# Kernel tuning notes

Measured on AMD Instinct MI355X. Metric: run time of the kernel, lower is better.

Reference implementation:

```python
import jax, jax.numpy as jnp
import numpy as np

B, T, IN, H, STEPS = 32768, 11, 2, 64, 80


def gru_cell(x, h, W_ih, W_hh, b_ih, b_hh):
    # PyTorch GRU cell: gates ordered (r, z, n)
    gi = x @ W_ih.T + b_ih            # [B, 3H]
    gh = h @ W_hh.T + b_hh            # [B, 3H]
    gi_r, gi_z, gi_n = jnp.split(gi, 3, axis=-1)
    gh_r, gh_z, gh_n = jnp.split(gh, 3, axis=-1)
    r = jax.nn.sigmoid(gi_r + gh_r)
    z = jax.nn.sigmoid(gi_z + gh_z)
    n = jnp.tanh(gi_n + r * gh_n)
    return (1.0 - z) * n + z * h


def setup_inputs() -> dict:
    key = jax.random.key(0)
    ks = jax.random.split(key, 20)
    s = 1.0 / np.sqrt(H)
    u = lambda k, shape: jax.random.uniform(k, shape, jnp.float32, -s, s)
    inp = {"x": jax.random.normal(ks[0], (B, T, IN), jnp.float32)}
    i = 1
    for pfx, in0 in (("e", IN), ("d", IN)):
        for l, d_in in ((0, in0), (1, H)):
            inp[f"{pfx}W_ih{l}"] = u(ks[i], (3 * H, d_in)); i += 1
            inp[f"{pfx}W_hh{l}"] = u(ks[i], (3 * H, H)); i += 1
            inp[f"{pfx}b_ih{l}"] = u(ks[i], (3 * H,)); i += 1
            inp[f"{pfx}b_hh{l}"] = u(ks[i], (3 * H,)); i += 1
    inp["fc_W"] = u(ks[17], (2, H))
    inp["fc_b"] = u(ks[18], (2,))
    return inp


def reference(x, eW_ih0, eW_hh0, eb_ih0, eb_hh0, eW_ih1, eW_hh1, eb_ih1, eb_hh1,
              dW_ih0, dW_hh0, db_ih0, db_hh0, dW_ih1, dW_hh1, db_ih1, db_hh1,
              fc_W, fc_b):
    b = x.shape[0]
    h0 = jnp.zeros((b, H), x.dtype)
    h1 = jnp.zeros((b, H), x.dtype)

    # ---- encoder: 2-layer GRU over time (dropout inactive in eval) ----
    def enc_step(carry, xt):
        c0, c1 = carry
        c0 = gru_cell(xt, c0, eW_ih0, eW_hh0, eb_ih0, eb_hh0)
        c1 = gru_cell(c0, c1, eW_ih1, eW_hh1, eb_ih1, eb_hh1)
        return (c0, c1), None

    (h0, h1), _ = jax.lax.scan(enc_step, (h0, h1), jnp.swapaxes(x, 0, 1))

    def dec_step(carry, _):
        inp, c0, c1 = carry
        c0 = gru_cell(inp, c0, dW_ih0, dW_hh0, db_ih0, db_hh0)
        c1 = gru_cell(c0, c1, dW_ih1, dW_hh1, db_ih1, db_hh1)
        pred = c1 @ fc_W.T + fc_b     # [B, 2]
        return (pred, c0, c1), pred

    init = (x[:, -1, :], h0, h1)
    _, preds = jax.lax.scan(dec_step, init, None, length=STEPS)  # [80, B, 2]
    return jnp.swapaxes(preds, 0, 1)  # [B, 80, 2]
```

## Files before the change

kernel.cpp:

```cpp
#include <hip/hip_runtime.h>
#include <cstddef>

#define T_SEQ 11
#define STEPS 80
#define SRC (-1.44269504f)
#define SNC ( 2.88539008f)

typedef _Float16 f16;
typedef _Float16 f16x4 __attribute__((ext_vector_type(4)));
typedef _Float16 f16x8 __attribute__((ext_vector_type(8)));
typedef float    f32x4 __attribute__((ext_vector_type(4)));

#define W0H   0
#define W1X   12288
#define WPADO 24576
#define HB    30720
#define BIASH 47104
#define LDS_BYTES (47104*2 + 512*4)

__device__ __forceinline__ f32x4 mfma16(f16x8 a, f16x8 b, f32x4 c) {
    return __builtin_amdgcn_mfma_f32_16x16x32_f16(a, b, c, 0, 0, 0);
}

__device__ __forceinline__ void stage_w(f16* lds, int dst, const float* __restrict__ W, int tid) {
    for (int c = tid; c < 1536; c += 512) {
        const int row = c >> 3, kc = c & 7;
        const float sc = (row < 128) ? SRC : SNC;
        const float* p = W + row * 64 + kc * 8;
        f16x8 v;
        #pragma unroll
        for (int i = 0; i < 8; ++i) v[i] = (f16)(sc * p[i]);
        *(f16x8*)(lds + dst + row * 64 + ((kc ^ (row & 7)) << 3)) = v;
    }
}
__device__ __forceinline__ void stage_pad(f16* lds, const float* __restrict__ Wih0, int tid) {
    for (int c = tid; c < 768; c += 512) {
        const int row = c >> 2, kc = c & 3;
        const float sc = (row < 128) ? SRC : SNC;
        f16x8 v;
        #pragma unroll
        for (int i = 0; i < 8; ++i) v[i] = (f16)0.f;
        if (kc == 0) { v[0] = (f16)(sc * Wih0[row * 2]); v[1] = (f16)(sc * Wih0[row * 2 + 1]); }
        *(f16x8*)(lds + WPADO + row * 32 + ((kc ^ (row & 3)) << 3)) = v;
    }
}
__device__ __forceinline__ void stage_bias(float* bb, int base, const float* __restrict__ bih,
                                           const float* __restrict__ bhh, int tid) {
    for (int t = tid; t < 256; t += 512) {
        const int a = t >> 6, j = t & 63;
        float v;
        if (a == 0)      v = SRC * (bih[j] + bhh[j]);
        else if (a == 1) v = SRC * (bih[64 + j] + bhh[64 + j]);
        else if (a == 2) v = SNC * bih[128 + j];
        else             v = SNC * bhh[128 + j];
        bb[(base + a) * 64 + j] = v;
    }
}

__device__ __forceinline__ f16x8 wfrag(const float* __restrict__ W, int row, int k0, float sc) {
    f16x8 r;
    #pragma unroll
    for (int i = 0; i < 8; ++i) r[i] = (f16)(sc * W[row * 64 + k0 + i]);
    return r;
}
__device__ __forceinline__ void load_wregs(f16x8 (&R)[8], f16x8 (&Z)[8], f16x8 (&N)[8],
                                           const float* __restrict__ Whh, int col, int quad) {
    #pragma unroll
    for (int ks = 0; ks < 2; ++ks) {
        #pragma unroll
        for (int mt = 0; mt < 4; ++mt) {
            const int k0 = ks * 32 + quad * 8;
            R[ks * 4 + mt] = wfrag(Whh, mt * 16 + col,       k0, SRC);
            Z[ks * 4 + mt] = wfrag(Whh, 64  + mt * 16 + col, k0, SRC);
            N[ks * 4 + mt] = wfrag(Whh, 128 + mt * 16 + col, k0, SNC);
        }
    }
}

struct Lane {
    int col, quad, c7, colr, x0, x1, xp;
    int wo[4];
};

__device__ __forceinline__ void cell_l0(f16* lds, const Lane& L, f16x4 (&ho)[4],
                                        f16x8 xpb, int h0off)
{
    const float* bb = (const float*)(lds + BIASH);
    f16x8 hb0 = *(const f16x8*)(lds + h0off + L.colr + L.x0);
    f16x8 hb1 = *(const f16x8*)(lds + h0off + L.colr + L.x1);
    #pragma unroll
    for (int mt = 0; mt < 4; ++mt) {
        const int bj = mt * 16 + L.quad * 4;
        f32x4 bR  = *(const f32x4*)(bb + 0 * 64 + bj);
        f32x4 bZ  = *(const f32x4*)(bb + 1 * 64 + bj);
        f32x4 bNi = *(const f32x4*)(bb + 2 * 64 + bj);
        f32x4 bNh = *(const f32x4*)(bb + 3 * 64 + bj);
        const int ar = (mt * 16 + L.col) * 64;
        f16x8 hR0 = *(const f16x8*)(lds + W0H        + ar + L.x0);
        f16x8 hR1 = *(const f16x8*)(lds + W0H        + ar + L.x1);
        f16x8 hZ0 = *(const f16x8*)(lds + W0H + 4096 + ar + L.x0);
        f16x8 hZ1 = *(const f16x8*)(lds + W0H + 4096 + ar + L.x1);
        f16x8 hN0 = *(const f16x8*)(lds + W0H + 8192 + ar + L.x0);
        f16x8 hN1 = *(const f16x8*)(lds + W0H + 8192 + ar + L.x1);
        const int pr = (mt * 16 + L.col) * 32;
        f16x8 pR = *(const f16x8*)(lds + WPADO        + pr + L.xp);
        f16x8 pZ = *(const f16x8*)(lds + WPADO + 2048 + pr + L.xp);
        f16x8 pN = *(const f16x8*)(lds + WPADO + 4096 + pr + L.xp);
        f32x4 aR  = mfma16(hR0, hb0, bR);  aR  = mfma16(hR1, hb1, aR);
        f32x4 aZ  = mfma16(hZ0, hb0, bZ);  aZ  = mfma16(hZ1, hb1, aZ);
        f32x4 aNh = mfma16(hN0, hb0, bNh); aNh = mfma16(hN1, hb1, aNh);
        aR  = mfma16(pR, xpb, aR);
        aZ  = mfma16(pZ, xpb, aZ);
        f32x4 aNi = mfma16(pN, xpb, bNi);
        f16x4 o;
        #pragma unroll
        for (int i = 0; i < 4; ++i) {
            const float r = __builtin_amdgcn_rcpf(1.f + __builtin_amdgcn_exp2f(aR[i]));
            const float z = __builtin_amdgcn_rcpf(1.f + __builtin_amdgcn_exp2f(aZ[i]));
            const float n = 1.f - 2.f * __builtin_amdgcn_rcpf(1.f + __builtin_amdgcn_exp2f(aNi[i] + r * aNh[i]));
            const float h = n + z * ((float)ho[mt][i] - n);
            o[i] = (f16)h;
        }
        ho[mt] = o;
        *(f16x4*)(lds + h0off + L.wo[mt]) = o;
    }
}

__device__ __forceinline__ void cell_l1(f16* lds, const Lane& L, f16x4 (&ho)[4],
    const f16x8 (&cR)[8], const f16x8 (&cZ)[8], const f16x8 (&cN)[8],
    int h0off, int h1off)
{
    const float* bb = (const float*)(lds + BIASH);
    f16x8 xb0 = *(const f16x8*)(lds + h0off + L.colr + L.x0);
    f16x8 xb1 = *(const f16x8*)(lds + h0off + L.colr + L.x1);
    f16x8 hb0 = *(const f16x8*)(lds + h1off + L.colr + L.x0);
    f16x8 hb1 = *(const f16x8*)(lds + h1off + L.colr + L.x1);
    #pragma unroll
    for (int mt = 0; mt < 4; ++mt) {
        const int bj = mt * 16 + L.quad * 4;
        f32x4 bR  = *(const f32x4*)(bb + 4 * 64 + bj);
        f32x4 bZ  = *(const f32x4*)(bb + 5 * 64 + bj);
        f32x4 bNi = *(const f32x4*)(bb + 6 * 64 + bj);
        f32x4 bNh = *(const f32x4*)(bb + 7 * 64 + bj);
        const int ar = (mt * 16 + L.col) * 64;
        f16x8 xR0 = *(const f16x8*)(lds + W1X        + ar + L.x0);
        f16x8 xR1 = *(const f16x8*)(lds + W1X        + ar + L.x1);
        f16x8 xZ0 = *(const f16x8*)(lds + W1X + 4096 + ar + L.x0);
        f16x8 xZ1 = *(const f16x8*)(lds + W1X + 4096 + ar + L.x1);
        f16x8 xN0 = *(const f16x8*)(lds + W1X + 8192 + ar + L.x0);
        f16x8 xN1 = *(const f16x8*)(lds + W1X + 8192 + ar + L.x1);
        f32x4 aR  = mfma16(cR[mt],     hb0, bR);
        f32x4 aZ  = mfma16(cZ[mt],     hb0, bZ);
        f32x4 aNh = mfma16(cN[mt],     hb0, bNh);
        aR  = mfma16(cR[4 + mt], hb1, aR);
        aZ  = mfma16(cZ[4 + mt], hb1, aZ);
        aNh = mfma16(cN[4 + mt], hb1, aNh);
        aR  = mfma16(xR0, xb0, aR);   aR  = mfma16(xR1, xb1, aR);
        aZ  = mfma16(xZ0, xb0, aZ);   aZ  = mfma16(xZ1, xb1, aZ);
        f32x4 aNi = mfma16(xN0, xb0, bNi); aNi = mfma16(xN1, xb1, aNi);
        f16x4 o;
        #pragma unroll
        for (int i = 0; i < 4; ++i) {
            const float r = __builtin_amdgcn_rcpf(1.f + __builtin_amdgcn_exp2f(aR[i]));
            const float z = __builtin_amdgcn_rcpf(1.f + __builtin_amdgcn_exp2f(aZ[i]));
            const float n = 1.f - 2.f * __builtin_amdgcn_rcpf(1.f + __builtin_amdgcn_exp2f(aNi[i] + r * aNh[i]));
            const float h = n + z * ((float)ho[mt][i] - n);
            o[i] = (f16)h;
        }
        ho[mt] = o;
        *(f16x4*)(lds + h1off + L.wo[mt]) = o;
    }
}

__global__ __launch_bounds__(512, 1)
void gru_wave3(
    const float* __restrict__ x,
    const float* __restrict__ eWih0, const float* __restrict__ eWhh0,
    const float* __restrict__ ebih0, const float* __restrict__ ebhh0,
    const float* __restrict__ eWih1, const float* __restrict__ eWhh1,
    const float* __restrict__ ebih1, const float* __restrict__ ebhh1,
    const float* __restrict__ dWih0, const float* __restrict__ dWhh0,
    const float* __restrict__ dbih0, const float* __restrict__ dbhh0,
    const float* __restrict__ dWih1, const float* __restrict__ dWhh1,
    const float* __restrict__ dbih1, const float* __restrict__ dbhh1,
    const float* __restrict__ fcW,  const float* __restrict__ fcb,
    float* __restrict__ out)
{
    extern __shared__ f16 lds[];
    float* bb = (float*)(lds + BIASH);
    const int tid  = threadIdx.x;
    const int lane = tid & 63;
    const int wv   = __builtin_amdgcn_readfirstlane(tid >> 6);

    Lane L;
    L.col  = lane & 15;
    L.quad = lane >> 4;
    L.c7   = L.col & 7;
    L.colr = L.col * 64;
    L.x0   = (L.quad ^ L.c7) << 3;
    L.x1   = ((4 + L.quad) ^ L.c7) << 3;
    L.xp   = (L.quad ^ (L.col & 3)) << 3;
    #pragma unroll
    for (int mt = 0; mt < 4; ++mt)
        L.wo[mt] = L.colr + (((2 * mt + (L.quad >> 1)) ^ L.c7) << 3) + ((L.quad & 1) << 2);

    const int r0    = blockIdx.x * 128;
    const int myrow = r0 + wv * 16 + L.col;
    const int h0off = HB + wv * 2048;
    const int h1off = h0off + 1024;

    stage_w(lds, W0H, eWhh0, tid);
    stage_w(lds, W1X, eWih1, tid);
    stage_pad(lds, eWih0, tid);
    stage_bias(bb, 0, ebih0, ebhh0, tid);
    stage_bias(bb, 4, ebih1, ebhh1, tid);
    {
        f16x8 z;
        #pragma unroll
        for (int i = 0; i < 8; ++i) z[i] = (f16)0.f;
        for (int k = lane; k < 256; k += 64) *(f16x8*)(lds + h0off + k * 8) = z;
    }
    f16x8 w1R[8], w1Z[8], w1N[8];
    load_wregs(w1R, w1Z, w1N, eWhh1, L.col, L.quad);
    f16x4 ho0[4], ho1[4];
    #pragma unroll
    for (int m = 0; m < 4; ++m) {
        #pragma unroll
        for (int i = 0; i < 4; ++i) { ho0[m][i] = (f16)0.f; ho1[m][i] = (f16)0.f; }
    }
    __syncthreads();

    const float* xrow = x + (size_t)myrow * (T_SEQ * 2);
    f16x8 zf;
    #pragma unroll
    for (int i = 0; i < 8; ++i) zf[i] = (f16)0.f;

    #pragma unroll 1
    for (int t = 0; t < T_SEQ; ++t) {
        const float2 xv = *(const float2*)(xrow + t * 2);
        f16x8 xpb = zf;
        if (L.quad == 0) { xpb[0] = (f16)xv.x; xpb[1] = (f16)xv.y; }
        cell_l0(lds, L, ho0, xpb, h0off);
        cell_l1(lds, L, ho1, w1R, w1Z, w1N, h0off, h1off);
    }

    __syncthreads();
    stage_w(lds, W0H, dWhh0, tid);
    stage_w(lds, W1X, dWih1, tid);
    stage_pad(lds, dWih0, tid);
    stage_bias(bb, 0, dbih0, dbhh0, tid);
    stage_bias(bb, 4, dbih1, dbhh1, tid);
    load_wregs(w1R, w1Z, w1N, dWhh1, L.col, L.quad);
    __syncthreads();

    f16x8 fcf0 = zf, fcf1 = zf;
    if (L.col < 2) {
        #pragma unroll
        for (int i = 0; i < 8; ++i) {
            fcf0[i] = (f16)fcW[L.col * 64 + L.quad * 8 + i];
            fcf1[i] = (f16)fcW[L.col * 64 + 32 + L.quad * 8 + i];
        }
    }
    f32x4 pb;
    #pragma unroll
    for (int rg = 0; rg < 4; ++rg) pb[rg] = (L.quad == 0 && rg < 2) ? fcb[rg] : 0.f;

    float* __restrict__ outp = out + (size_t)myrow * (STEPS * 2);

    f16x8 xpb = zf;
    {
        const float2 xv = *(const float2*)(xrow + (T_SEQ - 1) * 2);
        if (L.quad == 0) { xpb[0] = (f16)xv.x; xpb[1] = (f16)xv.y; }
    }

    #pragma unroll 1
    for (int s = 0; s < STEPS; ++s) {
        cell_l0(lds, L, ho0, xpb, h0off);
        cell_l1(lds, L, ho1, w1R, w1Z, w1N, h0off, h1off);
        f16x8 b0 = *(const f16x8*)(lds + h1off + L.colr + L.x0);
        f16x8 b1 = *(const f16x8*)(lds + h1off + L.colr + L.x1);
        f32x4 p = mfma16(fcf0, b0, pb);
        p = mfma16(fcf1, b1, p);
        xpb = zf;
        if (L.quad == 0) {
            *(float2*)(outp + s * 2) = make_float2(p[0], p[1]);
            xpb[0] = (f16)p[0];
            xpb[1] = (f16)p[1];
        }
    }
}

extern "C" void kernel_launch(void* const* d_in, const int* in_sizes, int n_in,
                              void* d_out, int out_size, void* d_ws, size_t ws_size,
                              hipStream_t stream) {
    (void)n_in; (void)out_size; (void)d_ws; (void)ws_size;

    const float* x     = (const float*)d_in[0];
    const float* eWih0 = (const float*)d_in[1];
    const float* eWhh0 = (const float*)d_in[2];
    const float* ebih0 = (const float*)d_in[3];
    const float* ebhh0 = (const float*)d_in[4];
    const float* eWih1 = (const float*)d_in[5];
    const float* eWhh1 = (const float*)d_in[6];
    const float* ebih1 = (const float*)d_in[7];
    const float* ebhh1 = (const float*)d_in[8];
    const float* dWih0 = (const float*)d_in[9];
    const float* dWhh0 = (const float*)d_in[10];
    const float* dbih0 = (const float*)d_in[11];
    const float* dbhh0 = (const float*)d_in[12];
    const float* dWih1 = (const float*)d_in[13];
    const float* dWhh1 = (const float*)d_in[14];
    const float* dbih1 = (const float*)d_in[15];
    const float* dbhh1 = (const float*)d_in[16];
    const float* fcW   = (const float*)d_in[17];
    const float* fcb   = (const float*)d_in[18];
    float* out = (float*)d_out;

    hipFuncSetAttribute((const void*)gru_wave3,
        hipFuncAttributeMaxDynamicSharedMemorySize, LDS_BYTES);

    const int b = in_sizes[0] / (T_SEQ * 2);
    dim3 grid(b / 128), block(512);
    hipLaunchKernelGGL(gru_wave3, grid, block, LDS_BYTES, stream,
        x, eWih0, eWhh0, ebih0, ebhh0, eWih1, eWhh1, ebih1, ebhh1,
        dWih0, dWhh0, dbih0, dbhh0, dWih1, dWhh1, dbih1, dbhh1,
        fcW, fcb, out);
}
```

Before: 480.9 us.

## Process two 16-row tiles per wave and keep layer-1 input weights in registers

Each wave now handles 32 batch rows as two 16-row N-tiles, so every weight fragment read from LDS feeds two MFMA chains. The block shrinks from 8 to 4 waves (256 threads) while still covering 128 rows. Layer-1 input weights move from LDS into registers alongside the recurrent weights, which frees LDS and removes those per-step LDS reads. This doubles register pressure for weights and state and halves the waves per CU, so there is less latency hiding and a risk of spills.

```diff
diff --git a/kernel.cpp b/kernel.cpp
--- a/kernel.cpp
+++ b/kernel.cpp
@@ -12,18 +12,17 @@
 typedef float    f32x4 __attribute__((ext_vector_type(4)));
 
 #define W0H   0
-#define W1X   12288
-#define WPADO 24576
-#define HB    30720
-#define BIASH 47104
-#define LDS_BYTES (47104*2 + 512*4)
+#define WPADO 12288
+#define HB    18432
+#define BIASH 34816
+#define LDS_BYTES (34816*2 + 512*4)
 
 __device__ __forceinline__ f32x4 mfma16(f16x8 a, f16x8 b, f32x4 c) {
     return __builtin_amdgcn_mfma_f32_16x16x32_f16(a, b, c, 0, 0, 0);
 }
 
 __device__ __forceinline__ void stage_w(f16* lds, int dst, const float* __restrict__ W, int tid) {
-    for (int c = tid; c < 1536; c += 512) {
+    for (int c = tid; c < 1536; c += 256) {
         const int row = c >> 3, kc = c & 7;
         const float sc = (row < 128) ? SRC : SNC;
         const float* p = W + row * 64 + kc * 8;
@@ -34,7 +33,7 @@
     }
 }
 __device__ __forceinline__ void stage_pad(f16* lds, const float* __restrict__ Wih0, int tid) {
-    for (int c = tid; c < 768; c += 512) {
+    for (int c = tid; c < 768; c += 256) {
         const int row = c >> 2, kc = c & 3;
         const float sc = (row < 128) ? SRC : SNC;
         f16x8 v;
@@ -46,7 +45,7 @@
 }
 __device__ __forceinline__ void stage_bias(float* bb, int base, const float* __restrict__ bih,
                                            const float* __restrict__ bhh, int tid) {
-    for (int t = tid; t < 256; t += 512) {
+    for (int t = tid; t < 256; t += 256) {
         const int a = t >> 6, j = t & 63;
         float v;
         if (a == 0)      v = SRC * (bih[j] + bhh[j]);
@@ -64,15 +63,15 @@
     return r;
 }
 __device__ __forceinline__ void load_wregs(f16x8 (&R)[8], f16x8 (&Z)[8], f16x8 (&N)[8],
-                                           const float* __restrict__ Whh, int col, int quad) {
+                                           const float* __restrict__ W, int col, int quad) {
     #pragma unroll
     for (int ks = 0; ks < 2; ++ks) {
         #pragma unroll
         for (int mt = 0; mt < 4; ++mt) {
             const int k0 = ks * 32 + quad * 8;
-            R[ks * 4 + mt] = wfrag(Whh, mt * 16 + col,       k0, SRC);
-            Z[ks * 4 + mt] = wfrag(Whh, 64  + mt * 16 + col, k0, SRC);
-            N[ks * 4 + mt] = wfrag(Whh, 128 + mt * 16 + col, k0, SNC);
+            R[ks * 4 + mt] = wfrag(W, mt * 16 + col,       k0, SRC);
+            Z[ks * 4 + mt] = wfrag(W, 64  + mt * 16 + col, k0, SRC);
+            N[ks * 4 + mt] = wfrag(W, 128 + mt * 16 + col, k0, SNC);
         }
     }
 }
@@ -82,12 +81,32 @@
     int wo[4];
 };
 
-__device__ __forceinline__ void cell_l0(f16* lds, const Lane& L, f16x4 (&ho)[4],
-                                        f16x8 xpb, int h0off)
+__device__ __forceinline__ void gates4(f32x4 aR, f32x4 aZ, f32x4 aNi, f32x4 aNh,
+                                       f16x4& ho, f16* dst)
+{
+    f16x4 o;
+    #pragma unroll
+    for (int i = 0; i < 4; ++i) {
+        const float r = __builtin_amdgcn_rcpf(1.f + __builtin_amdgcn_exp2f(aR[i]));
+        const float z = __builtin_amdgcn_rcpf(1.f + __builtin_amdgcn_exp2f(aZ[i]));
+        const float n = 1.f - 2.f * __builtin_amdgcn_rcpf(1.f + __builtin_amdgcn_exp2f(aNi[i] + r * aNh[i]));
+        const float h = n + z * ((float)ho[i] - n);
+        o[i] = (f16)h;
+    }
+    ho = o;
+    *(f16x4*)dst = o;
+}
+
+__device__ __forceinline__ void cell_l0(f16* lds, const Lane& L, f16x4 (&ho)[4][2],
+                                        const f16x8 (&xpb)[2], int h0b)
 {
     const float* bb = (const float*)(lds + BIASH);
-    f16x8 hb0 = *(const f16x8*)(lds + h0off + L.colr + L.x0);
-    f16x8 hb1 = *(const f16x8*)(lds + h0off + L.colr + L.x1);
+    f16x8 hb[2][2];
+    #pragma unroll
+    for (int nt = 0; nt < 2; ++nt) {
+        hb[nt][0] = *(const f16x8*)(lds + h0b + nt * 1024 + L.colr + L.x0);
+        hb[nt][1] = *(const f16x8*)(lds + h0b + nt * 1024 + L.colr + L.x1);
+    }
     #pragma unroll
     for (int mt = 0; mt < 4; ++mt) {
         const int bj = mt * 16 + L.quad * 4;
@@ -106,35 +125,33 @@
         f16x8 pR = *(const f16x8*)(lds + WPADO        + pr + L.xp);
         f16x8 pZ = *(const f16x8*)(lds + WPADO + 2048 + pr + L.xp);
         f16x8 pN = *(const f16x8*)(lds + WPADO + 4096 + pr + L.xp);
-        f32x4 aR  = mfma16(hR0, hb0, bR);  aR  = mfma16(hR1, hb1, aR);
-        f32x4 aZ  = mfma16(hZ0, hb0, bZ);  aZ  = mfma16(hZ1, hb1, aZ);
-        f32x4 aNh = mfma16(hN0, hb0, bNh); aNh = mfma16(hN1, hb1, aNh);
-        aR  = mfma16(pR, xpb, aR);
-        aZ  = mfma16(pZ, xpb, aZ);
-        f32x4 aNi = mfma16(pN, xpb, bNi);
-        f16x4 o;
-        #pragma unroll
-        for (int i = 0; i < 4; ++i) {
-            const float r = __builtin_amdgcn_rcpf(1.f + __builtin_amdgcn_exp2f(aR[i]));
-            const float z = __builtin_amdgcn_rcpf(1.f + __builtin_amdgcn_exp2f(aZ[i]));
-            const float n = 1.f - 2.f * __builtin_amdgcn_rcpf(1.f + __builtin_amdgcn_exp2f(aNi[i] + r * aNh[i]));
-            const float h = n + z * ((float)ho[mt][i] - n);
-            o[i] = (f16)h;
-        }
-        ho[mt] = o;
-        *(f16x4*)(lds + h0off + L.wo[mt]) = o;
-    }
-}
-
-__device__ __forceinline__ void cell_l1(f16* lds, const Lane& L, f16x4 (&ho)[4],
+        #pragma unroll
+        for (int nt = 0; nt < 2; ++nt) {
+            f32x4 aR  = mfma16(hR0, hb[nt][0], bR);  aR  = mfma16(hR1, hb[nt][1], aR);
+            f32x4 aZ  = mfma16(hZ0, hb[nt][0], bZ);  aZ  = mfma16(hZ1, hb[nt][1], aZ);
+            f32x4 aNh = mfma16(hN0, hb[nt][0], bNh); aNh = mfma16(hN1, hb[nt][1], aNh);
+            aR = mfma16(pR, xpb[nt], aR);
+            aZ = mfma16(pZ, xpb[nt], aZ);
+            f32x4 aNi = mfma16(pN, xpb[nt], bNi);
+            gates4(aR, aZ, aNi, aNh, ho[mt][nt], lds + h0b + nt * 1024 + L.wo[mt]);
+        }
+    }
+}
+
+__device__ __forceinline__ void cell_l1(f16* lds, const Lane& L, f16x4 (&ho)[4][2],
     const f16x8 (&cR)[8], const f16x8 (&cZ)[8], const f16x8 (&cN)[8],
-    int h0off, int h1off)
+    const f16x8 (&xR)[8], const f16x8 (&xZ)[8], const f16x8 (&xN)[8],
+    int h0b, int h1b)
 {
     const float* bb = (const float*)(lds + BIASH);
-    f16x8 xb0 = *(const f16x8*)(lds + h0off + L.colr + L.x0);
-    f16x8 xb1 = *(const f16x8*)(lds + h0off + L.colr + L.x1);
-    f16x8 hb0 = *(const f16x8*)(lds + h1off + L.colr + L.x0);
-    f16x8 hb1 = *(const f16x8*)(lds + h1off + L.colr + L.x1);
+    f16x8 xb[2][2], hv[2][2];
+    #pragma unroll
+    for (int nt = 0; nt < 2; ++nt) {
+        xb[nt][0] = *(const f16x8*)(lds + h0b + nt * 1024 + L.colr + L.x0);
+        xb[nt][1] = *(const f16x8*)(lds + h0b + nt * 1024 + L.colr + L.x1);
+        hv[nt][0] = *(const f16x8*)(lds + h1b + nt * 1024 + L.colr + L.x0);
+        hv[nt][1] = *(const f16x8*)(lds + h1b + nt * 1024 + L.colr + L.x1);
+    }
     #pragma unroll
     for (int mt = 0; mt < 4; ++mt) {
         const int bj = mt * 16 + L.quad * 4;
@@ -142,38 +159,27 @@
         f32x4 bZ  = *(const f32x4*)(bb + 5 * 64 + bj);
         f32x4 bNi = *(const f32x4*)(bb + 6 * 64 + bj);
         f32x4 bNh = *(const f32x4*)(bb + 7 * 64 + bj);
-        const int ar = (mt * 16 + L.col) * 64;
-        f16x8 xR0 = *(const f16x8*)(lds + W1X        + ar + L.x0);
-        f16x8 xR1 = *(const f16x8*)(lds + W1X        + ar + L.x1);
-        f16x8 xZ0 = *(const f16x8*)(lds + W1X + 4096 + ar + L.x0);
-        f16x8 xZ1 = *(const f16x8*)(lds + W1X + 4096 + ar + L.x1);
-        f16x8 xN0 = *(const f16x8*)(lds + W1X + 8192 + ar + L.x0);
-        f16x8 xN1 = *(const f16x8*)(lds + W1X + 8192 + ar + L.x1);
-        f32x4 aR  = mfma16(cR[mt],     hb0, bR);
-        f32x4 aZ  = mfma16(cZ[mt],     hb0, bZ);
-        f32x4 aNh = mfma16(cN[mt],     hb0, bNh);
-        aR  = mfma16(cR[4 + mt], hb1, aR);
-        aZ  = mfma16(cZ[4 + mt], hb1, aZ);
-        aNh = mfma16(cN[4 + mt], hb1, aNh);
-        aR  = mfma16(xR0, xb0, aR);   aR  = mfma16(xR1, xb1, aR);
-        aZ  = mfma16(xZ0, xb0, aZ);   aZ  = mfma16(xZ1, xb1, aZ);
-        f32x4 aNi = mfma16(xN0, xb0, bNi); aNi = mfma16(xN1, xb1, aNi);
-        f16x4 o;
-        #pragma unroll
-        for (int i = 0; i < 4; ++i) {
-            const float r = __builtin_amdgcn_rcpf(1.f + __builtin_amdgcn_exp2f(aR[i]));
-            const float z = __builtin_amdgcn_rcpf(1.f + __builtin_amdgcn_exp2f(aZ[i]));
-            const float n = 1.f - 2.f * __builtin_amdgcn_rcpf(1.f + __builtin_amdgcn_exp2f(aNi[i] + r * aNh[i]));
-            const float h = n + z * ((float)ho[mt][i] - n);
-            o[i] = (f16)h;
-        }
-        ho[mt] = o;
-        *(f16x4*)(lds + h1off + L.wo[mt]) = o;
-    }
-}
-
-__global__ __launch_bounds__(512, 1)
-void gru_wave3(
+        #pragma unroll
+        for (int nt = 0; nt < 2; ++nt) {
+            f32x4 aR  = mfma16(cR[mt], hv[nt][0], bR);
+            f32x4 aZ  = mfma16(cZ[mt], hv[nt][0], bZ);
+            f32x4 aNh = mfma16(cN[mt], hv[nt][0], bNh);
+            aR  = mfma16(cR[4 + mt], hv[nt][1], aR);
+            aZ  = mfma16(cZ[4 + mt], hv[nt][1], aZ);
+            aNh = mfma16(cN[4 + mt], hv[nt][1], aNh);
+            aR  = mfma16(xR[mt], xb[nt][0], aR);
+            aZ  = mfma16(xZ[mt], xb[nt][0], aZ);
+            f32x4 aNi = mfma16(xN[mt], xb[nt][0], bNi);
+            aR  = mfma16(xR[4 + mt], xb[nt][1], aR);
+            aZ  = mfma16(xZ[4 + mt], xb[nt][1], aZ);
+            aNi = mfma16(xN[4 + mt], xb[nt][1], aNi);
+            gates4(aR, aZ, aNi, aNh, ho[mt][nt], lds + h1b + nt * 1024 + L.wo[mt]);
+        }
+    }
+}
+
+__global__ __launch_bounds__(256, 1)
+void gru_wave4(
     const float* __restrict__ x,
     const float* __restrict__ eWih0, const float* __restrict__ eWhh0,
     const float* __restrict__ ebih0, const float* __restrict__ ebhh0,
@@ -204,13 +210,11 @@
     for (int mt = 0; mt < 4; ++mt)
         L.wo[mt] = L.colr + (((2 * mt + (L.quad >> 1)) ^ L.c7) << 3) + ((L.quad & 1) << 2);
 
-    const int r0    = blockIdx.x * 128;
-    const int myrow = r0 + wv * 16 + L.col;
-    const int h0off = HB + wv * 2048;
-    const int h1off = h0off + 1024;
+    const int rowb = blockIdx.x * 128 + wv * 32;
+    const int h0b  = HB + wv * 4096;
+    const int h1b  = h0b + 2048;
 
     stage_w(lds, W0H, eWhh0, tid);
-    stage_w(lds, W1X, eWih1, tid);
     stage_pad(lds, eWih0, tid);
     stage_bias(bb, 0, ebih0, ebhh0, tid);
     stage_bias(bb, 4, ebih1, ebhh1, tid);
@@ -218,39 +222,49 @@
         f16x8 z;
         #pragma unroll
         for (int i = 0; i < 8; ++i) z[i] = (f16)0.f;
-        for (int k = lane; k < 256; k += 64) *(f16x8*)(lds + h0off + k * 8) = z;
-    }
-    f16x8 w1R[8], w1Z[8], w1N[8];
-    load_wregs(w1R, w1Z, w1N, eWhh1, L.col, L.quad);
-    f16x4 ho0[4], ho1[4];
+        for (int k = lane; k < 512; k += 64) *(f16x8*)(lds + h0b + k * 8) = z;
+    }
+    f16x8 c1R[8], c1Z[8], c1N[8];
+    f16x8 x1R[8], x1Z[8], x1N[8];
+    load_wregs(c1R, c1Z, c1N, eWhh1, L.col, L.quad);
+    load_wregs(x1R, x1Z, x1N, eWih1, L.col, L.quad);
+    f16x4 ho0[4][2], ho1[4][2];
     #pragma unroll
     for (int m = 0; m < 4; ++m) {
         #pragma unroll
-        for (int i = 0; i < 4; ++i) { ho0[m][i] = (f16)0.f; ho1[m][i] = (f16)0.f; }
+        for (int nt = 0; nt < 2; ++nt) {
+            #pragma unroll
+            for (int i = 0; i < 4; ++i) { ho0[m][nt][i] = (f16)0.f; ho1[m][nt][i] = (f16)0.f; }
+        }
     }
     __syncthreads();
 
-    const float* xrow = x + (size_t)myrow * (T_SEQ * 2);
+    const float* xr0 = x + (size_t)(rowb + L.col) * (T_SEQ * 2);
+    const float* xr1 = x + (size_t)(rowb + 16 + L.col) * (T_SEQ * 2);
     f16x8 zf;
     #pragma unroll
     for (int i = 0; i < 8; ++i) zf[i] = (f16)0.f;
 
     #pragma unroll 1
     for (int t = 0; t < T_SEQ; ++t) {
-        const float2 xv = *(const float2*)(xrow + t * 2);
-        f16x8 xpb = zf;
-        if (L.quad == 0) { xpb[0] = (f16)xv.x; xpb[1] = (f16)xv.y; }
-        cell_l0(lds, L, ho0, xpb, h0off);
-        cell_l1(lds, L, ho1, w1R, w1Z, w1N, h0off, h1off);
+        f16x8 xpb[2] = {zf, zf};
+        if (L.quad == 0) {
+            const float2 a = *(const float2*)(xr0 + t * 2);
+            const float2 b = *(const float2*)(xr1 + t * 2);
+            xpb[0][0] = (f16)a.x; xpb[0][1] = (f16)a.y;
+            xpb[1][0] = (f16)b.x; xpb[1][1] = (f16)b.y;
+        }
+        cell_l0(lds, L, ho0, xpb, h0b);
+        cell_l1(lds, L, ho1, c1R, c1Z, c1N, x1R, x1Z, x1N, h0b, h1b);
     }
 
     __syncthreads();
     stage_w(lds, W0H, dWhh0, tid);
-    stage_w(lds, W1X, dWih1, tid);
     stage_pad(lds, dWih0, tid);
     stage_bias(bb, 0, dbih0, dbhh0, tid);
     stage_bias(bb, 4, dbih1, dbhh1, tid);
-    load_wregs(w1R, w1Z, w1N, dWhh1, L.col, L.quad);
+    load_wregs(c1R, c1Z, c1N, dWhh1, L.col, L.quad);
+    load_wregs(x1R, x1Z, x1N, dWih1, L.col, L.quad);
     __syncthreads();
 
     f16x8 fcf0 = zf, fcf1 = zf;
@@ -265,27 +279,34 @@
     #pragma unroll
     for (int rg = 0; rg < 4; ++rg) pb[rg] = (L.quad == 0 && rg < 2) ? fcb[rg] : 0.f;
 
-    float* __restrict__ outp = out + (size_t)myrow * (STEPS * 2);
-
-    f16x8 xpb = zf;
-    {
-        const float2 xv = *(const float2*)(xrow + (T_SEQ - 1) * 2);
-        if (L.quad == 0) { xpb[0] = (f16)xv.x; xpb[1] = (f16)xv.y; }
+    float* __restrict__ op0 = out + (size_t)(rowb + L.col) * (STEPS * 2);
+    float* __restrict__ op1 = out + (size_t)(rowb + 16 + L.col) * (STEPS * 2);
+
+    f16x8 xpb[2] = {zf, zf};
+    if (L.quad == 0) {
+        const float2 a = *(const float2*)(xr0 + (T_SEQ - 1) * 2);
+        const float2 b = *(const float2*)(xr1 + (T_SEQ - 1) * 2);
+        xpb[0][0] = (f16)a.x; xpb[0][1] = (f16)a.y;
+        xpb[1][0] = (f16)b.x; xpb[1][1] = (f16)b.y;
     }
 
     #pragma unroll 1
     for (int s = 0; s < STEPS; ++s) {
-        cell_l0(lds, L, ho0, xpb, h0off);
-        cell_l1(lds, L, ho1, w1R, w1Z, w1N, h0off, h1off);
-        f16x8 b0 = *(const f16x8*)(lds + h1off + L.colr + L.x0);
-        f16x8 b1 = *(const f16x8*)(lds + h1off + L.colr + L.x1);
-        f32x4 p = mfma16(fcf0, b0, pb);
-        p = mfma16(fcf1, b1, p);
-        xpb = zf;
-        if (L.quad == 0) {
-            *(float2*)(outp + s * 2) = make_float2(p[0], p[1]);
-            xpb[0] = (f16)p[0];
-            xpb[1] = (f16)p[1];
+        cell_l0(lds, L, ho0, xpb, h0b);
+        cell_l1(lds, L, ho1, c1R, c1Z, c1N, x1R, x1Z, x1N, h0b, h1b);
+        #pragma unroll
+        for (int nt = 0; nt < 2; ++nt) {
+            f16x8 b0 = *(const f16x8*)(lds + h1b + nt * 1024 + L.colr + L.x0);
+            f16x8 b1 = *(const f16x8*)(lds + h1b + nt * 1024 + L.colr + L.x1);
+            f32x4 p = mfma16(fcf0, b0, pb);
+            p = mfma16(fcf1, b1, p);
+            xpb[nt] = zf;
+            if (L.quad == 0) {
+                float* op = nt ? op1 : op0;
+                *(float2*)(op + s * 2) = make_float2(p[0], p[1]);
+                xpb[nt][0] = (f16)p[0];
+                xpb[nt][1] = (f16)p[1];
+            }
         }
     }
 }
@@ -316,12 +337,12 @@
     const float* fcb   = (const float*)d_in[18];
     float* out = (float*)d_out;
 
-    hipFuncSetAttribute((const void*)gru_wave3,
+    hipFuncSetAttribute((const void*)gru_wave4,
         hipFuncAttributeMaxDynamicSharedMemorySize, LDS_BYTES);
 
     const int b = in_sizes[0] / (T_SEQ * 2);
-    dim3 grid(b / 128), block(512);
-    hipLaunchKernelGGL(gru_wave3, grid, block, LDS_BYTES, stream,
+    dim3 grid(b / 128), block(256);
+    hipLaunchKernelGGL(gru_wave4, grid, block, LDS_BYTES, stream,
         x, eWih0, eWhh0, ebih0, ebhh0, eWih1, eWhh1, ebih1, ebhh1,
         dWih0, dWhh0, dbih0, dbhh0, dWih1, dWhh1, dbih1, dbhh1,
         fcW, fcb, out);
```

Result: slower. 569.3 us (+18.4%).
